# Optimization experiments

Measured on AMD Instinct MI355X. Metric: run time of the kernel, lower is better.

The kernel has to match this reference:

```python
import jax, jax.numpy as jnp
import numpy as np

B, T, F, H = 64, 512, 1024, 1024

def setup_inputs() -> dict:
    key = jax.random.key(0)
    k1, k2, k3 = jax.random.split(key, 3)
    x = jax.random.normal(k1, (B, T, F), dtype=jnp.float32)
    # fused gate kernels, flax gate order: i, f, g, o
    Wx = jax.random.normal(k2, (F, 4 * H), dtype=jnp.float32) / np.sqrt(F).astype(np.float32)
    Wh = jax.random.normal(k3, (H, 4 * H), dtype=jnp.float32) / np.sqrt(H).astype(np.float32)
    b = jnp.zeros((4 * H,), dtype=jnp.float32)
    return {"x": x, "Wx": Wx, "Wh": Wh, "b": b}

def reference(x, Wx, Wh, b):
    """Unidirectional LSTM matching flax OptimizedLSTMCell scanned over axis 1.

    x: [B, T, F] -> hs: [B, T, H]
    """
    Bb = x.shape[0]
    Hh = Wh.shape[0]
    # Precompute the input projection for all timesteps (same math, one big GEMM).
    xg = jnp.einsum('btf,fg->btg', x, Wx)  # [B, T, 4H]

    def step(carry, xt):
        c, h = carry
        z = xt + h @ Wh + b                     # [B, 4H]
        i, f, g, o = jnp.split(z, 4, axis=-1)   # flax gate order i,f,g,o
        new_c = jax.nn.sigmoid(f) * c + jax.nn.sigmoid(i) * jnp.tanh(g)
        new_h = jax.nn.sigmoid(o) * jnp.tanh(new_c)
        return (new_c, new_h), new_h

    c0 = jnp.zeros((Bb, Hh), dtype=x.dtype)
    h0 = jnp.zeros((Bb, Hh), dtype=x.dtype)
    (_, _), hs = jax.lax.scan(step, (c0, h0), jnp.swapaxes(xg, 0, 1))  # time-major scan
    return jnp.swapaxes(hs, 0, 1)  # [B, T, H]
```

## Files before the change

kernel.cpp:

```cpp
#include <hip/hip_runtime.h>
#include <hip/hip_bf16.h>
#include <stdint.h>

typedef __bf16 bf16x8 __attribute__((ext_vector_type(8)));
typedef float  floatx4 __attribute__((ext_vector_type(4)));

static constexpr int kT = 512, kH = 1024, k4H = 4096;

__global__ void pack_w(const float* __restrict__ Wx, const float* __restrict__ Wh,
                       __bf16* __restrict__ wpk) {
  int idx = blockIdx.x * 256 + threadIdx.x;
  int l  = idx & 63;
  int c  = (idx >> 6) & 63;
  int np = idx >> 12;
  int nl = l & 15;
  int g  = nl & 3, hl = nl >> 2;
  int col = g * kH + np * 4 + hl;
  int kf  = (l >> 4) * 8;
  const float* src = (c < 32) ? Wx + (size_t)(c * 32 + kf) * k4H + col
                              : Wh + (size_t)((c - 32) * 32 + kf) * k4H + col;
  bf16x8 v;
#pragma unroll
  for (int j = 0; j < 8; ++j) v[j] = (__bf16)src[(size_t)j * k4H];
  *(bf16x8*)(wpk + (size_t)idx * 8) = v;
}

__global__ void pack_x(const float* __restrict__ x, __bf16* __restrict__ xpk) {
  int idx = blockIdx.x * 256 + threadIdx.x;
  int l  = idx & 63;
  int c  = (idx >> 6) & 31;
  int mt = (idx >> 11) & 3;
  int t  = idx >> 13;
  int m  = mt * 16 + (l & 15);
  int f  = c * 32 + (l >> 4) * 8;
  const float4* src = (const float4*)(x + ((size_t)m * kT + t) * 1024 + f);
  float4 r0 = src[0], r1 = src[1];
  bf16x8 v;
  v[0] = (__bf16)r0.x; v[1] = (__bf16)r0.y; v[2] = (__bf16)r0.z; v[3] = (__bf16)r0.w;
  v[4] = (__bf16)r1.x; v[5] = (__bf16)r1.y; v[6] = (__bf16)r1.z; v[7] = (__bf16)r1.w;
  *(bf16x8*)(xpk + (size_t)idx * 8) = v;
}

__launch_bounds__(512, 2)
__global__ void lstm_scan(const __bf16* __restrict__ xpk, const __bf16* __restrict__ wpk,
                          const float* __restrict__ bias, uint32_t* __restrict__ hd,
                          int* __restrict__ sent, float* __restrict__ out) {
  const int blk  = blockIdx.x;
  const int half = blk & 1;
  const int mq   = (blk >> 1) & 3;
  const int cg   = half * 32 + (blk >> 3);
  const int tid  = threadIdx.x;
  const int wave = tid >> 6;
  const int lane = tid & 63;

  __shared__ __align__(16) float zbuf[8][16][68];

  bf16x8 breg[4][8];
#pragma unroll
  for (int nt = 0; nt < 4; ++nt) {
    const __bf16* wsrc = wpk + (((size_t)(cg * 4 + nt) * 64 + wave * 8) * 64 + lane) * 8;
#pragma unroll
    for (int cc = 0; cc < 8; ++cc)
      breg[nt][cc] = *(const bf16x8*)(wsrc + (size_t)cc * 512);
  }
#pragma unroll
  for (int nt = 0; nt < 4; ++nt)
#pragma unroll
    for (int cc = 0; cc < 8; ++cc)
      asm volatile("" : "+v"(breg[nt][cc]));

  const int gm   = (tid >> 4) & 15;
  const int ghc  = tid & 15;
  const int m_g  = mq * 16 + gm;
  const int hcol = cg * 16 + ghc;
  const int gnt  = ghc >> 2, ghl = ghc & 3;
  float c_state  = 0.f;
  float h_keep   = 0.f;
  const float bi = bias[0 * kH + hcol], bf_ = bias[1 * kH + hcol];
  const float bg = bias[2 * kH + hcol], bo  = bias[3 * kH + hcol];
  const int hdoff = ((mq * 128 + cg * 2 + (ghc >> 3)) * 16 + gm) * 4 + ((ghc & 7) >> 1);

  floatx4 acc[4];
#pragma unroll
  for (int nt = 0; nt < 4; ++nt) acc[nt] = floatx4{0.f, 0.f, 0.f, 0.f};

  if (wave < 4) {
    const __bf16* asrc = xpk + ((size_t)mq * 32 + wave * 8) * 512 + (size_t)lane * 8;
#pragma unroll
    for (int cc = 0; cc < 8; ++cc) {
      bf16x8 a = *(const bf16x8*)(asrc + (size_t)cc * 512);
#pragma unroll
      for (int nt = 0; nt < 4; ++nt)
        acc[nt] = __builtin_amdgcn_mfma_f32_16x16x32_bf16(a, breg[nt][cc], acc[nt], 0, 0, 0);
    }
  }

#pragma unroll 1
  for (int t = 0; t < kT; ++t) {
#pragma unroll
    for (int nt = 0; nt < 4; ++nt)
#pragma unroll
      for (int rr = 0; rr < 4; ++rr)
        zbuf[wave][(lane >> 4) * 4 + rr][nt * 16 + (lane & 15)] = acc[nt][rr];
    __syncthreads();

    if (tid < 256) {
      float zi = bi, zf = bf_, zg = bg, zo = bo;
      const float* zp = &zbuf[0][gm][gnt * 16 + ghl * 4];
#pragma unroll
      for (int w = 0; w < 8; ++w) {
        floatx4 zv = *(const floatx4*)(zp + (size_t)w * 16 * 68);
        zi += zv[0]; zf += zv[1]; zg += zv[2]; zo += zv[3];
      }
      float ig = 1.f / (1.f + __expf(-zi));
      float fg = 1.f / (1.f + __expf(-zf));
      float gg = 2.f / (1.f + __expf(-2.f * zg)) - 1.f;
      float og = 1.f / (1.f + __expf(-zo));
      c_state = fg * c_state + ig * gg;
      float tc = 2.f / (1.f + __expf(-2.f * c_state)) - 1.f;
      float h  = og * tc;
      h_keep = h;
      __bf16 hb16 = (__bf16)h;
      uint16_t hbits;
      __builtin_memcpy(&hbits, &hb16, 2);
      uint32_t mine = hbits;
      uint32_t partner = (uint32_t)__shfl_xor((int)mine, 1);
      if ((ghc & 1) == 0) {
        uint32_t packed = mine | (partner << 16);
        __hip_atomic_store(&hd[(size_t)(t & 3) * 32768 + hdoff], packed,
                           __ATOMIC_RELAXED, __HIP_MEMORY_SCOPE_AGENT);
      }
    }
    __syncthreads();

    if (tid == 0)
      __hip_atomic_store(&sent[(((t & 7) * 4 + mq) * 4 + (cg >> 4)) * 16 + (cg & 15)], t,
                         __ATOMIC_RELAXED, __HIP_MEMORY_SCOPE_AGENT);

    if (wave < 4)
      out[((size_t)m_g * kT + t) * kH + hcol] = h_keep;

    if (t < kT - 1) {
#pragma unroll
      for (int nt = 0; nt < 4; ++nt) acc[nt] = floatx4{0.f, 0.f, 0.f, 0.f};
      if (wave < 4) {
        const __bf16* asrc = xpk + (((size_t)(t + 1) * 4 + mq) * 32 + wave * 8) * 512
                           + (size_t)lane * 8;
#pragma unroll
        for (int cc = 0; cc < 8; ++cc) {
          bf16x8 a = __builtin_nontemporal_load((const bf16x8*)(asrc + (size_t)cc * 512));
#pragma unroll
          for (int nt = 0; nt < 4; ++nt)
            acc[nt] = __builtin_amdgcn_mfma_f32_16x16x32_bf16(a, breg[nt][cc], acc[nt], 0, 0, 0);
        }
      } else {
        const int s = wave - 4;
        const int* sline = sent + (((t & 7) * 4 + mq) * 4 + s) * 16 + (lane & 15);
        int guard = 0;
        for (;;) {
          int v = __hip_atomic_load(sline, __ATOMIC_RELAXED, __HIP_MEMORY_SCOPE_AGENT);
          if (__all(v == t)) break;
          __builtin_amdgcn_s_sleep(2);
          if (++guard > (1 << 20)) break;
        }
        asm volatile("" ::: "memory");
        const uint64_t* hb = (const uint64_t*)hd + (size_t)(t & 3) * 16384
                           + ((size_t)(mq * 128 + s * 32 + (lane >> 4)) * 16 + (lane & 15)) * 2;
        uint64_t w[8][2];
#pragma unroll
        for (int c = 0; c < 8; ++c) {
          w[c][0] = __hip_atomic_load(hb + (size_t)c * 128,     __ATOMIC_RELAXED,
                                      __HIP_MEMORY_SCOPE_AGENT);
          w[c][1] = __hip_atomic_load(hb + (size_t)c * 128 + 1, __ATOMIC_RELAXED,
                                      __HIP_MEMORY_SCOPE_AGENT);
        }
#pragma unroll
        for (int c = 0; c < 8; ++c) {
          union { uint64_t q[2]; bf16x8 v; } u;
          u.q[0] = w[c][0]; u.q[1] = w[c][1];
#pragma unroll
          for (int nt = 0; nt < 4; ++nt)
            acc[nt] = __builtin_amdgcn_mfma_f32_16x16x32_bf16(u.v, breg[nt][c], acc[nt], 0, 0, 0);
        }
      }
    }
  }
}

extern "C" void kernel_launch(void* const* d_in, const int* in_sizes, int n_in,
                              void* d_out, int out_size, void* d_ws, size_t ws_size,
                              hipStream_t stream) {
  const float* x  = (const float*)d_in[0];
  const float* Wx = (const float*)d_in[1];
  const float* Wh = (const float*)d_in[2];
  const float* b  = (const float*)d_in[3];
  float* out = (float*)d_out;

  char* ws = (char*)d_ws;
  int*      snt = (int*)ws;
  uint32_t* hdb = (uint32_t*)(ws + ((size_t)1 << 16));
  __bf16*   wpk = (__bf16*)(ws + ((size_t)1 << 20));
  __bf16*   xpk = (__bf16*)(ws + ((size_t)17 << 20));
  (void)in_sizes; (void)n_in; (void)out_size; (void)ws_size;

  hipLaunchKernelGGL(pack_w, dim3(4096),  dim3(256), 0, stream, Wx, Wh, wpk);
  hipLaunchKernelGGL(pack_x, dim3(16384), dim3(256), 0, stream, x, xpk);
  hipLaunchKernelGGL(lstm_scan, dim3(256), dim3(512), 0, stream,
                     xpk, wpk, b, hdb, snt, out);
}
```

Measured before the change: 1.895 ms.

## Use a 512-slot bit-reversed h ring buffer with plain vector loads

When the workspace is large enough, the hidden-state exchange buffer grows from 4 to 512 regions, indexed by bit-reversed timestep. Each step therefore writes to a fresh address, so consumers can use ordinary 128-bit vector loads instead of per-64-bit agent-scope atomic loads without reading stale cached lines. The aim is to cut the cost and latency of loading h on the recurrent critical path. This relies on no cache line being reused within a run; repeated calls reuse the same regions and could read stale data unless caches are invalidated between launches, and the larger footprint may hurt cache locality.

After: 1.746 ms. 7.9% less time.

```diff
diff --git a/kernel.cpp b/kernel.cpp
--- a/kernel.cpp
+++ b/kernel.cpp
@@ -4,6 +4,7 @@
 
 typedef __bf16 bf16x8 __attribute__((ext_vector_type(8)));
 typedef float  floatx4 __attribute__((ext_vector_type(4)));
+typedef unsigned int uint32x4 __attribute__((ext_vector_type(4)));
 
 static constexpr int kT = 512, kH = 1024, k4H = 4096;
 
@@ -41,6 +42,7 @@
   *(bf16x8*)(xpk + (size_t)idx * 8) = v;
 }
 
+template<int BIGRING>
 __launch_bounds__(512, 2)
 __global__ void lstm_scan(const __bf16* __restrict__ xpk, const __bf16* __restrict__ wpk,
                           const float* __restrict__ bias, uint32_t* __restrict__ hd,
@@ -97,6 +99,8 @@
 
 #pragma unroll 1
   for (int t = 0; t < kT; ++t) {
+    const int region = BIGRING ? (int)(__brev((unsigned)t) >> 23) : (t & 3);
+
 #pragma unroll
     for (int nt = 0; nt < 4; ++nt)
 #pragma unroll
@@ -127,7 +131,7 @@
       uint32_t partner = (uint32_t)__shfl_xor((int)mine, 1);
       if ((ghc & 1) == 0) {
         uint32_t packed = mine | (partner << 16);
-        __hip_atomic_store(&hd[(size_t)(t & 3) * 32768 + hdoff], packed,
+        __hip_atomic_store(&hd[(size_t)region * 32768 + hdoff], packed,
                            __ATOMIC_RELAXED, __HIP_MEMORY_SCOPE_AGENT);
       }
     }
@@ -164,15 +168,24 @@
           if (++guard > (1 << 20)) break;
         }
         asm volatile("" ::: "memory");
-        const uint64_t* hb = (const uint64_t*)hd + (size_t)(t & 3) * 16384
+        const uint64_t* hb = (const uint64_t*)hd + (size_t)region * 16384
                            + ((size_t)(mq * 128 + s * 32 + (lane >> 4)) * 16 + (lane & 15)) * 2;
         uint64_t w[8][2];
-#pragma unroll
-        for (int c = 0; c < 8; ++c) {
-          w[c][0] = __hip_atomic_load(hb + (size_t)c * 128,     __ATOMIC_RELAXED,
-                                      __HIP_MEMORY_SCOPE_AGENT);
-          w[c][1] = __hip_atomic_load(hb + (size_t)c * 128 + 1, __ATOMIC_RELAXED,
-                                      __HIP_MEMORY_SCOPE_AGENT);
+        if (BIGRING) {
+#pragma unroll
+          for (int c = 0; c < 8; ++c) {
+            uint32x4 ld = *(const uint32x4*)(hb + (size_t)c * 128);
+            w[c][0] = (uint64_t)ld.x | ((uint64_t)ld.y << 32);
+            w[c][1] = (uint64_t)ld.z | ((uint64_t)ld.w << 32);
+          }
+        } else {
+#pragma unroll
+          for (int c = 0; c < 8; ++c) {
+            w[c][0] = __hip_atomic_load(hb + (size_t)c * 128,     __ATOMIC_RELAXED,
+                                        __HIP_MEMORY_SCOPE_AGENT);
+            w[c][1] = __hip_atomic_load(hb + (size_t)c * 128 + 1, __ATOMIC_RELAXED,
+                                        __HIP_MEMORY_SCOPE_AGENT);
+          }
         }
 #pragma unroll
         for (int c = 0; c < 8; ++c) {
@@ -195,16 +208,29 @@
   const float* Wh = (const float*)d_in[2];
   const float* b  = (const float*)d_in[3];
   float* out = (float*)d_out;
+  (void)in_sizes; (void)n_in; (void)out_size;
 
   char* ws = (char*)d_ws;
-  int*      snt = (int*)ws;
-  uint32_t* hdb = (uint32_t*)(ws + ((size_t)1 << 16));
-  __bf16*   wpk = (__bf16*)(ws + ((size_t)1 << 20));
-  __bf16*   xpk = (__bf16*)(ws + ((size_t)17 << 20));
-  (void)in_sizes; (void)n_in; (void)out_size; (void)ws_size;
-
-  hipLaunchKernelGGL(pack_w, dim3(4096),  dim3(256), 0, stream, Wx, Wh, wpk);
-  hipLaunchKernelGGL(pack_x, dim3(16384), dim3(256), 0, stream, x, xpk);
-  hipLaunchKernelGGL(lstm_scan, dim3(256), dim3(512), 0, stream,
-                     xpk, wpk, b, hdb, snt, out);
-}
+  const size_t big_need = (size_t)0x10000 + ((size_t)64 << 20) + ((size_t)16 << 20)
+                        + ((size_t)64 << 20);
+
+  if (ws_size >= big_need) {
+    int*      snt = (int*)ws;
+    uint32_t* hdb = (uint32_t*)(ws + (size_t)0x10000);
+    __bf16*   wpk = (__bf16*)(ws + (size_t)0x10000 + ((size_t)64 << 20));
+    __bf16*   xpk = (__bf16*)(ws + (size_t)0x10000 + ((size_t)80 << 20));
+    hipLaunchKernelGGL(pack_w, dim3(4096),  dim3(256), 0, stream, Wx, Wh, wpk);
+    hipLaunchKernelGGL(pack_x, dim3(16384), dim3(256), 0, stream, x, xpk);
+    hipLaunchKernelGGL(lstm_scan<1>, dim3(256), dim3(512), 0, stream,
+                       xpk, wpk, b, hdb, snt, out);
+  } else {
+    int*      snt = (int*)ws;
+    uint32_t* hdb = (uint32_t*)(ws + ((size_t)1 << 16));
+    __bf16*   wpk = (__bf16*)(ws + ((size_t)1 << 20));
+    __bf16*   xpk = (__bf16*)(ws + ((size_t)17 << 20));
+    hipLaunchKernelGGL(pack_w, dim3(4096),  dim3(256), 0, stream, Wx, Wh, wpk);
+    hipLaunchKernelGGL(pack_x, dim3(16384), dim3(256), 0, stream, x, xpk);
+    hipLaunchKernelGGL(lstm_scan<0>, dim3(256), dim3(512), 0, stream,
+                       xpk, wpk, b, hdb, snt, out);
+  }
+}
```
